# Optimization experiments

Hardware: AMD Instinct MI355X
Metric: run time of the kernel (lower is better)

## Reference

```python
import jax, jax.numpy as jnp
import numpy as np

B, S, D = 8, 2048, 512
EPS = float(jnp.finfo(jnp.float32).eps)  # torch RMSNorm eps=None -> finfo eps


def rmsnorm(x, w):
    var = jnp.mean(jnp.square(x), axis=-1, keepdims=True)
    return x * jax.lax.rsqrt(var + EPS) * w


def setup_inputs() -> dict:
    key = jax.random.key(0)
    ks = jax.random.split(key, 9)
    x = jax.random.normal(ks[0], (B, S, D), dtype=jnp.float32)
    q_expl = jax.random.normal(ks[1], (B, S, D), dtype=jnp.float32)
    k_expl = jax.random.normal(ks[2], (B, S, D), dtype=jnp.float32)
    # parameters (torch Linear: y = x @ W^T + b; store W already transposed [in, out])
    sc1 = 1.0 / np.sqrt(D)
    W1 = jax.random.uniform(ks[3], (D, 2 * D), jnp.float32, -sc1, sc1)
    b1 = jax.random.uniform(ks[4], (2 * D,), jnp.float32, -sc1, sc1)
    W2 = jax.random.uniform(ks[5], (D, D), jnp.float32, -sc1, sc1)
    b2 = jax.random.uniform(ks[6], (D,), jnp.float32, -sc1, sc1)
    norm1_w = jnp.ones((D,), jnp.float32)
    norm2_w = jnp.ones((D,), jnp.float32)
    return {"x": x, "q_expl": q_expl, "k_expl": k_expl,
            "W1": W1, "b1": b1, "W2": W2, "b2": b2,
            "norm1_w": norm1_w, "norm2_w": norm2_w}


def reference(x, q_expl, k_expl, W1, b1, W2, b2, norm1_w, norm2_w):
    d = x.shape[-1]
    # single-head attention: scores [B,S,S]
    scores = jnp.einsum('bqd,bkd->bqk', q_expl, k_expl) / jnp.sqrt(jnp.float32(d))
    attn = jax.nn.softmax(scores, axis=-1)
    attn_out = jnp.einsum('bqk,bkd->bqd', attn, x)
    # dropout is identity in eval mode
    h = rmsnorm(x + attn_out, norm1_w)
    # GeGLU FFN: Linear(D->2D), chunk, gelu(x1)*x2, Linear(D->D)
    proj = h @ W1 + b1
    x1, x2 = jnp.split(proj, 2, axis=-1)
    g = jax.nn.gelu(x1, approximate=False) * x2
    ff = g @ W2 + b2
    return rmsnorm(h + ff, norm2_w)
```

## Files before the change

kernel.cpp:

```cpp
#include <hip/hip_runtime.h>
#include <math.h>

static constexpr float EPS_F = 1.1920929e-07f;
static constexpr float SCL   = 0.044194173824159216f;

typedef __attribute__((ext_vector_type(8))) short  short8;
typedef __attribute__((ext_vector_type(4))) float  floatx4;

__device__ __forceinline__ float4 ld4(const float* p){ return *(const float4*)p; }
__device__ __forceinline__ ushort f2bf(float f){
  union { float f; unsigned u; } v; v.f = f;
  return (ushort)((v.u + 0x7FFFu + ((v.u >> 16) & 1u)) >> 16);
}
__device__ __forceinline__ float bf2f(ushort h){
  union { unsigned u; float f; } v; v.u = ((unsigned)h) << 16;
  return v.f;
}
#define MFMA16(A,B,C) __builtin_amdgcn_mfma_f32_16x16x32_bf16((A),(B),(C),0,0,0)

__device__ __forceinline__ void gld16(void* lds, const void* g){
  __builtin_amdgcn_global_load_lds(
      (const __attribute__((address_space(1))) unsigned int*)g,
      (__attribute__((address_space(3))) unsigned int*)lds, 16, 0, 0);
}


__global__ __launch_bounds__(256)
void prep(const float* __restrict__ q, const float* __restrict__ k,
          const float* __restrict__ x, const float* __restrict__ W1,
          const float* __restrict__ W2,
          ushort* __restrict__ Qb, ushort* __restrict__ Kb,
          ushort* __restrict__ XT, ushort* __restrict__ W1T,
          ushort* __restrict__ W2T)
{
  const int bi = blockIdx.x, t = threadIdx.x;
  if (bi < 8192){
    const size_t i4 = ((size_t)bi*256 + t)*4;
    float4 v = ld4(q + i4);
    ushort4 o;
    o.x=f2bf(v.x*SCL); o.y=f2bf(v.y*SCL); o.z=f2bf(v.z*SCL); o.w=f2bf(v.w*SCL);
    *(ushort4*)(Qb + i4) = o;
    float4 u = ld4(k + i4);
    o.x=f2bf(u.x); o.y=f2bf(u.y); o.z=f2bf(u.z); o.w=f2bf(u.w);
    *(ushort4*)(Kb + i4) = o;
    return;
  }
  const float* in; ushort* out; int R, C, c0, r0; size_t boff;
  if (bi < 10240){
    const int id = bi - 8192;
    in = x; out = XT; R = 2048; C = 512;
    boff = (size_t)(id >> 8) * R * C;
    c0 = (id & 7)*64; r0 = ((id >> 3) & 31)*64;
  } else if (bi < 10368){
    const int id = bi - 10240;
    in = W1; out = W1T; R = 512; C = 1024; boff = 0;
    c0 = (id & 15)*64; r0 = (id >> 4)*64;
  } else {
    const int id = bi - 10368;
    in = W2; out = W2T; R = 512; C = 512; boff = 0;
    c0 = (id & 7)*64; r0 = (id >> 3)*64;
  }
  __shared__ __align__(16) ushort tile[64*68];
#pragma unroll
  for (int it = 0; it < 4; ++it){
    int f = t + it*256, r = f >> 4, c4 = f & 15;
    float4 v = ld4(in + boff + (size_t)(r0+r)*C + c0 + c4*4);
    ushort4 o; o.x=f2bf(v.x); o.y=f2bf(v.y); o.z=f2bf(v.z); o.w=f2bf(v.w);
    *(ushort4*)&tile[r*68 + c4*4] = o;
  }
  __syncthreads();
#pragma unroll
  for (int it = 0; it < 4; ++it){
    int f = t + it*256, c = f >> 4, q4 = f & 15;
    ushort4 o;
    o.x = tile[(q4*4+0)*68 + c];
    o.y = tile[(q4*4+1)*68 + c];
    o.z = tile[(q4*4+2)*68 + c];
    o.w = tile[(q4*4+3)*68 + c];
    *(ushort4*)(out + boff + (size_t)(c0+c)*R + r0 + q4*4) = o;
  }
}

__global__ __launch_bounds__(256)
void qk_gemm(const ushort* __restrict__ Qbf, const ushort* __restrict__ Kbf,
             ushort* __restrict__ scores, float* __restrict__ rowsum)
{
  __shared__ __align__(16) ushort As[2][128*32];
  __shared__ __align__(16) ushort Bs[2][128*32];
  const int t=threadIdx.x, lane=t&63, w=t>>6;
  const int id = blockIdx.x;
  const int b = id & 7, s = id >> 3;
  const int m0 = (s & 15)*128, n0 = (s >> 4)*128;
  const ushort* Qb = Qbf + ((size_t)b*2048 + m0)*512;
  const ushort* Kb = Kbf + ((size_t)b*2048 + n0)*512;
  const int sr = w*32 + (lane>>2), sc = (lane&3)*8;
  const int ga=(w&1)*4, gb2=(w>>1)*4, l15=lane&15, quad=lane>>4;

  floatx4 acc[4][4];
#pragma unroll
  for (int i=0;i<4;++i)
#pragma unroll
    for (int j=0;j<4;++j) acc[i][j]=(floatx4){0.f,0.f,0.f,0.f};

  auto stage = [&](int buf, int k0){
    gld16(&As[buf][(w*32)*32],    Qb + (size_t)sr*512      + k0 + sc);
    gld16(&As[buf][(w*32+16)*32], Qb + (size_t)(sr+16)*512 + k0 + sc);
    gld16(&Bs[buf][(w*32)*32],    Kb + (size_t)sr*512      + k0 + sc);
    gld16(&Bs[buf][(w*32+16)*32], Kb + (size_t)(sr+16)*512 + k0 + sc);
  };

  stage(0, 0);
  for (int kc=0; kc<16; ++kc){
    __syncthreads();
    if (kc < 15) stage((kc+1)&1, (kc+1)*32);
    const ushort* A = As[kc&1];
    const ushort* B = Bs[kc&1];
    short8 af[4], bfr[4];
#pragma unroll
    for (int i=0;i<4;++i) af[i]  = *(const short8*)&A[((ga+i)*16 + l15)*32 + quad*8];
#pragma unroll
    for (int j=0;j<4;++j) bfr[j] = *(const short8*)&B[((gb2+j)*16 + l15)*32 + quad*8];
#pragma unroll
    for (int i=0;i<4;++i)
#pragma unroll
      for (int j=0;j<4;++j)
        acc[i][j] = MFMA16(af[i], bfr[j], acc[i][j]);
  }

  ushort* sb = scores + (size_t)b*2048*2048;
  float rs[4][4];
#pragma unroll
  for (int i=0;i<4;++i)
#pragma unroll
    for (int r=0;r<4;++r) rs[i][r] = 0.f;
#pragma unroll
  for (int i=0;i<4;++i){
    const int rm = m0 + (ga+i)*16 + quad*4;
#pragma unroll
    for (int j=0;j<4;++j){
      const int cn = n0 + (gb2+j)*16 + l15;
#pragma unroll
      for (int r=0;r<4;++r){
        float e = __expf(acc[i][j][r]);
        ushort eb = f2bf(e);
        sb[(size_t)(rm+r)*2048 + cn] = eb;
        rs[i][r] += bf2f(eb);
      }
    }
  }
#pragma unroll
  for (int i=0;i<4;++i)
#pragma unroll
    for (int r=0;r<4;++r){
      float p = rs[i][r];
      p += __shfl_xor(p,1); p += __shfl_xor(p,2);
      p += __shfl_xor(p,4); p += __shfl_xor(p,8);
      if (l15 == 0)
        atomicAdd(&rowsum[(size_t)b*2048 + m0 + (ga+i)*16 + quad*4 + r], p);
    }
}

__global__ __launch_bounds__(256)
void pv128(const ushort* __restrict__ P, const ushort* __restrict__ XT,
           const float* __restrict__ rowsum, ushort* __restrict__ attn)
{
  __shared__ __align__(16) ushort As[2][128*32];
  __shared__ __align__(16) ushort Bs[2][128*32];
  const int t=threadIdx.x, lane=t&63, w=t>>6;
  const int id = blockIdx.x;
  const int b = id & 7, s = id >> 3;
  const int m0 = (s >> 2)*128, n0 = (s & 3)*128;
  const ushort* Pb = P  + ((size_t)b*2048 + m0)*2048;
  const ushort* Xb = XT + ((size_t)b*512  + n0)*2048;
  const int sr = w*32 + (lane>>2), sc = (lane&3)*8;
  const int ga=(w&1)*4, gb2=(w>>1)*4, l15=lane&15, quad=lane>>4;

  floatx4 acc[4][4];
#pragma unroll
  for (int i=0;i<4;++i)
#pragma unroll
    for (int j=0;j<4;++j) acc[i][j]=(floatx4){0.f,0.f,0.f,0.f};

  auto stage = [&](int buf, int k0){
    gld16(&As[buf][(w*32)*32],    Pb + (size_t)sr*2048      + k0 + sc);
    gld16(&As[buf][(w*32+16)*32], Pb + (size_t)(sr+16)*2048 + k0 + sc);
    gld16(&Bs[buf][(w*32)*32],    Xb + (size_t)sr*2048      + k0 + sc);
    gld16(&Bs[buf][(w*32+16)*32], Xb + (size_t)(sr+16)*2048 + k0 + sc);
  };

  stage(0, 0);
  for (int kc=0; kc<64; ++kc){
    __syncthreads();
    if (kc < 63) stage((kc+1)&1, (kc+1)*32);
    const ushort* A = As[kc&1];
    const ushort* B = Bs[kc&1];
    short8 af[4], bfr[4];
#pragma unroll
    for (int i=0;i<4;++i) af[i]  = *(const short8*)&A[((ga+i)*16 + l15)*32 + quad*8];
#pragma unroll
    for (int j=0;j<4;++j) bfr[j] = *(const short8*)&B[((gb2+j)*16 + l15)*32 + quad*8];
#pragma unroll
    for (int i=0;i<4;++i)
#pragma unroll
      for (int j=0;j<4;++j)
        acc[i][j] = MFMA16(af[i], bfr[j], acc[i][j]);
  }

  ushort* ab = attn + (size_t)b*2048*512;
#pragma unroll
  for (int i=0;i<4;++i){
    const int rm = m0 + (ga+i)*16 + quad*4;
    float inv[4];
#pragma unroll
    for (int r=0;r<4;++r)
      inv[r] = 1.0f / rowsum[(size_t)b*2048 + rm + r];
#pragma unroll
    for (int j=0;j<4;++j){
      const int cn = n0 + (gb2+j)*16 + l15;
#pragma unroll
      for (int r=0;r<4;++r)
        ab[(size_t)(rm+r)*512 + cn] = f2bf(acc[i][j][r] * inv[r]);
    }
  }
}

__global__ __launch_bounds__(256)
void res_rms1(const float* __restrict__ x, const float* __restrict__ n1w,
              ushort* __restrict__ ah)
{
  const int wid = threadIdx.x >> 6, lane = threadIdx.x & 63;
  const size_t row = (size_t)blockIdx.x*4 + wid;
  ushort* ar = ah + row*512;
  const float* xr = x + row*512;
  ushort4 a0 = *(const ushort4*)&ar[lane*8];
  ushort4 a1 = *(const ushort4*)&ar[lane*8 + 4];
  float4 x0 = ld4(xr + lane*8), x1 = ld4(xr + lane*8 + 4);
  float h[8];
  h[0]=x0.x+bf2f(a0.x); h[1]=x0.y+bf2f(a0.y); h[2]=x0.z+bf2f(a0.z); h[3]=x0.w+bf2f(a0.w);
  h[4]=x1.x+bf2f(a1.x); h[5]=x1.y+bf2f(a1.y); h[6]=x1.z+bf2f(a1.z); h[7]=x1.w+bf2f(a1.w);
  float ss = 0.f;
#pragma unroll
  for (int e=0;e<8;++e) ss += h[e]*h[e];
#pragma unroll
  for (int s=1;s<64;s<<=1) ss += __shfl_xor(ss, s);
  const float rr = rsqrtf(ss*(1.0f/512.0f) + EPS_F);
  ushort4 o0, o1;
  o0.x=f2bf(h[0]*rr*n1w[lane*8+0]); o0.y=f2bf(h[1]*rr*n1w[lane*8+1]);
  o0.z=f2bf(h[2]*rr*n1w[lane*8+2]); o0.w=f2bf(h[3]*rr*n1w[lane*8+3]);
  o1.x=f2bf(h[4]*rr*n1w[lane*8+4]); o1.y=f2bf(h[5]*rr*n1w[lane*8+5]);
  o1.z=f2bf(h[6]*rr*n1w[lane*8+6]); o1.w=f2bf(h[7]*rr*n1w[lane*8+7]);
  *(ushort4*)&ar[lane*8]     = o0;
  *(ushort4*)&ar[lane*8 + 4] = o1;
}

__global__ __launch_bounds__(256)
void ffn1(const ushort* __restrict__ hbf, const ushort* __restrict__ W1T,
          const float* __restrict__ b1, ushort* __restrict__ gbuf)
{
  __shared__ __align__(16) ushort As[2][128*32];
  __shared__ __align__(16) ushort Bs[2][128*32];
  const int t=threadIdx.x, lane=t&63, w=t>>6;
  const int id = blockIdx.x;
  const int xcd = id & 7, sl = id >> 3;
  const int m0 = (xcd*16 + (sl>>3))*128, n0 = (sl & 7)*64;
  const int sr = w*32 + (lane>>2), sc=(lane&3)*8;
  const int ga=(w&1)*4, b2w=(w>>1);
  const int l15=lane&15, quad=lane>>4;
  const int gr0 = (sr < 64) ? (n0+sr) : (448+n0+sr);
  const int sr1 = sr+16;
  const int gr1 = (sr1 < 64) ? (n0+sr1) : (448+n0+sr1);

  floatx4 acc[4][4];
#pragma unroll
  for (int i=0;i<4;++i)
#pragma unroll
    for (int j=0;j<4;++j) acc[i][j]=(floatx4){0.f,0.f,0.f,0.f};

  auto stage = [&](int buf, int k0){
    gld16(&As[buf][(w*32)*32],    hbf + (size_t)(m0+sr)*512  + k0 + sc);
    gld16(&As[buf][(w*32+16)*32], hbf + (size_t)(m0+sr1)*512 + k0 + sc);
    gld16(&Bs[buf][(w*32)*32],    W1T + (size_t)gr0*512 + k0 + sc);
    gld16(&Bs[buf][(w*32+16)*32], W1T + (size_t)gr1*512 + k0 + sc);
  };

  stage(0, 0);
  for (int kc=0; kc<16; ++kc){
    __syncthreads();
    if (kc < 15) stage((kc+1)&1, (kc+1)*32);
    const ushort* A = As[kc&1];
    const ushort* B = Bs[kc&1];
    short8 af[4], bfr[4];
#pragma unroll
    for (int i=0;i<4;++i) af[i] = *(const short8*)&A[((ga+i)*16 + l15)*32 + quad*8];
#pragma unroll
    for (int jj=0;jj<4;++jj){
      const int g1 = (jj<2) ? (b2w*2+jj) : (4 + b2w*2 + (jj-2));
      bfr[jj] = *(const short8*)&B[(g1*16 + l15)*32 + quad*8];
    }
#pragma unroll
    for (int i=0;i<4;++i)
#pragma unroll
      for (int jj=0;jj<4;++jj)
        acc[i][jj] = MFMA16(af[i], bfr[jj], acc[i][jj]);
  }

#pragma unroll
  for (int i=0;i<4;++i){
#pragma unroll
    for (int jj=0;jj<2;++jj){
      const int col = n0 + (b2w*2+jj)*16 + l15;
      const float bb1 = b1[col], bb2 = b1[512+col];
#pragma unroll
      for (int r=0;r<4;++r){
        const int row = m0 + (ga+i)*16 + quad*4 + r;
        float x1 = acc[i][jj][r]   + bb1;
        float x2 = acc[i][jj+2][r] + bb2;
        float gl = 0.5f*x1*(1.0f + erff(x1*0.70710678118654752f));
        gbuf[(size_t)row*512 + col] = f2bf(gl*x2);
      }
    }
  }
}

__global__ __launch_bounds__(256)
void ff128(const ushort* __restrict__ gb, const ushort* __restrict__ W2T,
           ushort* __restrict__ ff)
{
  __shared__ __align__(16) ushort As[2][128*32];
  __shared__ __align__(16) ushort Bs[2][128*32];
  const int t=threadIdx.x, lane=t&63, w=t>>6;
  const int id = blockIdx.x;
  const int xcd = id & 7, sl = id >> 3;
  const int m0 = (xcd*16 + (sl>>2))*128, n0 = (sl & 3)*128;
  const ushort* Ab = gb  + (size_t)m0*512;
  const ushort* Bb = W2T + (size_t)n0*512;
  const int sr = w*32 + (lane>>2), sc = (lane&3)*8;
  const int ga=(w&1)*4, gb2=(w>>1)*4, l15=lane&15, quad=lane>>4;

  floatx4 acc[4][4];
#pragma unroll
  for (int i=0;i<4;++i)
#pragma unroll
    for (int j=0;j<4;++j) acc[i][j]=(floatx4){0.f,0.f,0.f,0.f};

  auto stage = [&](int buf, int k0){
    gld16(&As[buf][(w*32)*32],    Ab + (size_t)sr*512      + k0 + sc);
    gld16(&As[buf][(w*32+16)*32], Ab + (size_t)(sr+16)*512 + k0 + sc);
    gld16(&Bs[buf][(w*32)*32],    Bb + (size_t)sr*512      + k0 + sc);
    gld16(&Bs[buf][(w*32+16)*32], Bb + (size_t)(sr+16)*512 + k0 + sc);
  };

  stage(0, 0);
  for (int kc=0; kc<16; ++kc){
    __syncthreads();
    if (kc < 15) stage((kc+1)&1, (kc+1)*32);
    const ushort* A = As[kc&1];
    const ushort* B = Bs[kc&1];
    short8 af[4], bfr[4];
#pragma unroll
    for (int i=0;i<4;++i) af[i]  = *(const short8*)&A[((ga+i)*16 + l15)*32 + quad*8];
#pragma unroll
    for (int j=0;j<4;++j) bfr[j] = *(const short8*)&B[((gb2+j)*16 + l15)*32 + quad*8];
#pragma unroll
    for (int i=0;i<4;++i)
#pragma unroll
      for (int j=0;j<4;++j)
        acc[i][j] = MFMA16(af[i], bfr[j], acc[i][j]);
  }

#pragma unroll
  for (int i=0;i<4;++i){
    const int rm = m0 + (ga+i)*16 + quad*4;
#pragma unroll
    for (int j=0;j<4;++j){
      const int cn = n0 + (gb2+j)*16 + l15;
#pragma unroll
      for (int r=0;r<4;++r)
        ff[(size_t)(rm+r)*512 + cn] = f2bf(acc[i][j][r]);
    }
  }
}

__global__ __launch_bounds__(256)
void res_rms2(const ushort* __restrict__ hbf, const ushort* __restrict__ ff,
              const float* __restrict__ b2, const float* __restrict__ n2w,
              float* __restrict__ out)
{
  const int wid = threadIdx.x >> 6, lane = threadIdx.x & 63;
  const size_t row = (size_t)blockIdx.x*4 + wid;
  const ushort* hr = hbf + row*512;
  const ushort* fr = ff  + row*512;
  ushort4 h0 = *(const ushort4*)&hr[lane*8];
  ushort4 h1 = *(const ushort4*)&hr[lane*8 + 4];
  ushort4 f0 = *(const ushort4*)&fr[lane*8];
  ushort4 f1 = *(const ushort4*)&fr[lane*8 + 4];
  float4 bb0 = ld4(b2 + lane*8), bb1 = ld4(b2 + lane*8 + 4);
  float y[8];
  y[0]=bf2f(h0.x)+bf2f(f0.x)+bb0.x; y[1]=bf2f(h0.y)+bf2f(f0.y)+bb0.y;
  y[2]=bf2f(h0.z)+bf2f(f0.z)+bb0.z; y[3]=bf2f(h0.w)+bf2f(f0.w)+bb0.w;
  y[4]=bf2f(h1.x)+bf2f(f1.x)+bb1.x; y[5]=bf2f(h1.y)+bf2f(f1.y)+bb1.y;
  y[6]=bf2f(h1.z)+bf2f(f1.z)+bb1.z; y[7]=bf2f(h1.w)+bf2f(f1.w)+bb1.w;
  float ss = 0.f;
#pragma unroll
  for (int e=0;e<8;++e) ss += y[e]*y[e];
#pragma unroll
  for (int s=1;s<64;s<<=1) ss += __shfl_xor(ss, s);
  const float rr = rsqrtf(ss*(1.0f/512.0f) + EPS_F);
  float4 w0 = ld4(n2w + lane*8), w1 = ld4(n2w + lane*8 + 4);
  float* orow = out + row*512;
  float4 o0, o1;
  o0.x=y[0]*rr*w0.x; o0.y=y[1]*rr*w0.y; o0.z=y[2]*rr*w0.z; o0.w=y[3]*rr*w0.w;
  o1.x=y[4]*rr*w1.x; o1.y=y[5]*rr*w1.y; o1.z=y[6]*rr*w1.z; o1.w=y[7]*rr*w1.w;
  *(float4*)(orow + lane*8)     = o0;
  *(float4*)(orow + lane*8 + 4) = o1;
}

extern "C" void kernel_launch(void* const* d_in, const int* in_sizes, int n_in,
                              void* d_out, int out_size, void* d_ws, size_t ws_size,
                              hipStream_t stream)
{
  const float* x   = (const float*)d_in[0];
  const float* q   = (const float*)d_in[1];
  const float* k   = (const float*)d_in[2];
  const float* W1  = (const float*)d_in[3];
  const float* b1  = (const float*)d_in[4];
  const float* W2  = (const float*)d_in[5];
  const float* b2  = (const float*)d_in[6];
  const float* n1w = (const float*)d_in[7];
  const float* n2w = (const float*)d_in[8];
  float* out = (float*)d_out;

  ushort* scoresP = (ushort*)d_ws;
  ushort* XT  = scoresP + (size_t)8*2048*2048;
  ushort* Qbf = XT  + (size_t)8*512*2048;
  ushort* Kbf = Qbf + (size_t)8*2048*512;
  ushort* W1T = Kbf + (size_t)8*2048*512;
  ushort* W2T = W1T + (size_t)1024*512;
  float*  rowsum = (float*)(W2T + (size_t)512*512);
  ushort* attn = Qbf;
  ushort* hbf  = Qbf;
  ushort* gbuf = Kbf;
  ushort* ffb  = scoresP;

  hipMemsetAsync(rowsum, 0, (size_t)8*2048*sizeof(float), stream);
  prep     <<<dim3(10432),  256, 0, stream>>>(q, k, x, W1, W2, Qbf, Kbf, XT, W1T, W2T);
  qk_gemm  <<<dim3(2048),   256, 0, stream>>>(Qbf, Kbf, scoresP, rowsum);
  pv128    <<<dim3(512),    256, 0, stream>>>(scoresP, XT, rowsum, attn);
  res_rms1 <<<dim3(4096),   256, 0, stream>>>(x, n1w, hbf);
  ffn1     <<<dim3(1024),   256, 0, stream>>>(hbf, W1T, b1, gbuf);
  ff128    <<<dim3(512),    256, 0, stream>>>(gbuf, W2T, ffb);
  res_rms2 <<<dim3(4096),   256, 0, stream>>>(hbf, ffb, b2, n2w, out);
}
```

Before: 340.8 us.

## Replace QK GEMM with 256x256-tile, 8-wave kernel using swizzled LDS pipeline

Replaces the 128x128-tile QK^T kernel with a 256x256-tile kernel of 512 threads (8 waves), each wave computing a 128x64 sub-tile, with a 64-wide K step and 128 KB of dynamic LDS. LDS rows are XOR-swizzled to avoid bank conflicts, and loads for the next tiles are issued in phases inside the MFMA loop, with explicit waitcnt, barriers and setprio. The goal is more operand reuse per byte loaded and better overlap of global loads with MFMA work. The cost is one block per CU, because of the large LDS footprint, and heavier register pressure from 32 accumulator tiles per wave.

```diff
diff --git a/kernel.cpp b/kernel.cpp
--- a/kernel.cpp
+++ b/kernel.cpp
@@ -23,7 +23,6 @@
       (const __attribute__((address_space(1))) unsigned int*)g,
       (__attribute__((address_space(3))) unsigned int*)lds, 16, 0, 0);
 }
-
 
 __global__ __launch_bounds__(256)
 void prep(const float* __restrict__ q, const float* __restrict__ k,
@@ -81,83 +80,120 @@
   }
 }
 
-__global__ __launch_bounds__(256)
-void qk_gemm(const ushort* __restrict__ Qbf, const ushort* __restrict__ Kbf,
-             ushort* __restrict__ scores, float* __restrict__ rowsum)
-{
-  __shared__ __align__(16) ushort As[2][128*32];
-  __shared__ __align__(16) ushort Bs[2][128*32];
-  const int t=threadIdx.x, lane=t&63, w=t>>6;
+__global__ __launch_bounds__(512)
+void qk8(const ushort* __restrict__ Qbf, const ushort* __restrict__ Kbf,
+         ushort* __restrict__ scores, float* __restrict__ rowsum)
+{
+  extern __shared__ __align__(16) ushort smem[];
+  const int t = threadIdx.x, lane = t & 63, w = t >> 6;
   const int id = blockIdx.x;
   const int b = id & 7, s = id >> 3;
-  const int m0 = (s & 15)*128, n0 = (s >> 4)*128;
-  const ushort* Qb = Qbf + ((size_t)b*2048 + m0)*512;
-  const ushort* Kb = Kbf + ((size_t)b*2048 + n0)*512;
-  const int sr = w*32 + (lane>>2), sc = (lane&3)*8;
-  const int ga=(w&1)*4, gb2=(w>>1)*4, l15=lane&15, quad=lane>>4;
-
-  floatx4 acc[4][4];
-#pragma unroll
-  for (int i=0;i<4;++i)
-#pragma unroll
-    for (int j=0;j<4;++j) acc[i][j]=(floatx4){0.f,0.f,0.f,0.f};
-
-  auto stage = [&](int buf, int k0){
-    gld16(&As[buf][(w*32)*32],    Qb + (size_t)sr*512      + k0 + sc);
-    gld16(&As[buf][(w*32+16)*32], Qb + (size_t)(sr+16)*512 + k0 + sc);
-    gld16(&Bs[buf][(w*32)*32],    Kb + (size_t)sr*512      + k0 + sc);
-    gld16(&Bs[buf][(w*32+16)*32], Kb + (size_t)(sr+16)*512 + k0 + sc);
+  const int m0 = (s & 7) * 256, n0 = (s >> 3) * 256;
+  const ushort* Qb = Qbf + ((size_t)b*2048 + (size_t)m0)*512;
+  const ushort* Kb = Kbf + ((size_t)b*2048 + (size_t)n0)*512;
+  const int wr = w >> 2, wc = w & 3;
+  const int l15 = lane & 15, quad = lane >> 4;
+  const int c0  = (quad ^ (l15 & 7)) * 8;
+  const int srow = lane >> 3;
+  const int skc  = ((lane & 7) ^ srow) * 8;
+
+  floatx4 acc[8][4];
+#pragma unroll
+  for (int i = 0; i < 8; ++i)
+#pragma unroll
+    for (int j = 0; j < 4; ++j) acc[i][j] = (floatx4){0.f,0.f,0.f,0.f};
+
+  auto stage = [&](int buf, const ushort* gsrc, int isB, int kt, int h){
+    ushort* base = smem + buf*32768 + isB*16384 + h*8192;
+#pragma unroll
+    for (int r = 0; r < 2; ++r){
+      const int rw = r*8 + w;
+      gld16(base + rw*512,
+            gsrc + (size_t)(h*128 + rw*8 + srow)*512 + kt*64 + skc);
+    }
   };
 
-  stage(0, 0);
-  for (int kc=0; kc<16; ++kc){
-    __syncthreads();
-    if (kc < 15) stage((kc+1)&1, (kc+1)*32);
-    const ushort* A = As[kc&1];
-    const ushort* B = Bs[kc&1];
-    short8 af[4], bfr[4];
-#pragma unroll
-    for (int i=0;i<4;++i) af[i]  = *(const short8*)&A[((ga+i)*16 + l15)*32 + quad*8];
-#pragma unroll
-    for (int j=0;j<4;++j) bfr[j] = *(const short8*)&B[((gb2+j)*16 + l15)*32 + quad*8];
-#pragma unroll
-    for (int i=0;i<4;++i)
-#pragma unroll
-      for (int j=0;j<4;++j)
-        acc[i][j] = MFMA16(af[i], bfr[j], acc[i][j]);
+  stage(0, Qb, 0, 0, 0);
+  stage(0, Qb, 0, 0, 1);
+  stage(0, Kb, 1, 0, 0);
+  stage(0, Kb, 1, 0, 1);
+  stage(1, Kb, 1, 1, 0);
+  stage(1, Kb, 1, 1, 1);
+  asm volatile("s_waitcnt vmcnt(4)" ::: "memory");
+  __builtin_amdgcn_s_barrier();
+
+  short8 af[2][2], bfr[4][2];
+  const int NT = 8;
+
+  for (int kt = 0; kt < NT; ++kt){
+    const int cur = kt & 1;
+    const ushort* A  = smem + cur*32768;
+    const ushort* Bt = A + 16384;
+#pragma unroll
+    for (int p = 0; p < 4; ++p){
+      if (p == 0){
+#pragma unroll
+        for (int ni = 0; ni < 4; ++ni)
+#pragma unroll
+          for (int ks = 0; ks < 2; ++ks)
+            bfr[ni][ks] = *(const short8*)
+              &Bt[(wc*64 + ni*16 + l15)*64 + (c0 ^ (ks*32))];
+      }
+#pragma unroll
+      for (int mi = 0; mi < 2; ++mi)
+#pragma unroll
+        for (int ks = 0; ks < 2; ++ks)
+          af[mi][ks] = *(const short8*)
+            &A[(wr*128 + (p*2 + mi)*16 + l15)*64 + (c0 ^ (ks*32))];
+      if (p == 0 && kt+1 < NT) stage(cur^1, Qb, 0, kt+1, 0);
+      if (p == 1 && kt+1 < NT) stage(cur^1, Qb, 0, kt+1, 1);
+      if (p == 2 && kt+2 < NT) stage(cur,   Kb, 1, kt+2, 0);
+      if (p == 3 && kt+2 < NT) stage(cur,   Kb, 1, kt+2, 1);
+      __builtin_amdgcn_s_barrier();
+      asm volatile("s_waitcnt lgkmcnt(0)" ::: "memory");
+      __builtin_amdgcn_sched_barrier(0);
+      __builtin_amdgcn_s_setprio(1);
+#pragma unroll
+      for (int mi = 0; mi < 2; ++mi)
+#pragma unroll
+        for (int ni = 0; ni < 4; ++ni)
+#pragma unroll
+          for (int ks = 0; ks < 2; ++ks)
+            acc[p*2+mi][ni] = MFMA16(af[mi][ks], bfr[ni][ks], acc[p*2+mi][ni]);
+      __builtin_amdgcn_s_setprio(0);
+      if (p == 3){
+        if (kt + 2 < NT) asm volatile("s_waitcnt vmcnt(4)" ::: "memory");
+        else             asm volatile("s_waitcnt vmcnt(0)" ::: "memory");
+      }
+      __builtin_amdgcn_s_barrier();
+    }
   }
 
   ushort* sb = scores + (size_t)b*2048*2048;
-  float rs[4][4];
-#pragma unroll
-  for (int i=0;i<4;++i)
-#pragma unroll
-    for (int r=0;r<4;++r) rs[i][r] = 0.f;
-#pragma unroll
-  for (int i=0;i<4;++i){
-    const int rm = m0 + (ga+i)*16 + quad*4;
-#pragma unroll
-    for (int j=0;j<4;++j){
-      const int cn = n0 + (gb2+j)*16 + l15;
-#pragma unroll
-      for (int r=0;r<4;++r){
-        float e = __expf(acc[i][j][r]);
+#pragma unroll
+  for (int m = 0; m < 8; ++m){
+    const int rm = m0 + wr*128 + m*16 + quad*4;
+    float rs[4] = {0.f,0.f,0.f,0.f};
+#pragma unroll
+    for (int n = 0; n < 4; ++n){
+      const int cn = n0 + wc*64 + n*16 + l15;
+#pragma unroll
+      for (int r = 0; r < 4; ++r){
+        float e = __expf(acc[m][n][r]);
         ushort eb = f2bf(e);
-        sb[(size_t)(rm+r)*2048 + cn] = eb;
-        rs[i][r] += bf2f(eb);
+        sb[(size_t)(rm + r)*2048 + cn] = eb;
+        rs[r] += bf2f(eb);
       }
     }
-  }
-#pragma unroll
-  for (int i=0;i<4;++i)
-#pragma unroll
-    for (int r=0;r<4;++r){
-      float p = rs[i][r];
-      p += __shfl_xor(p,1); p += __shfl_xor(p,2);
-      p += __shfl_xor(p,4); p += __shfl_xor(p,8);
+#pragma unroll
+    for (int r = 0; r < 4; ++r){
+      float p2 = rs[r];
+      p2 += __shfl_xor(p2, 1); p2 += __shfl_xor(p2, 2);
+      p2 += __shfl_xor(p2, 4); p2 += __shfl_xor(p2, 8);
       if (l15 == 0)
-        atomicAdd(&rowsum[(size_t)b*2048 + m0 + (ga+i)*16 + quad*4 + r], p);
-    }
+        atomicAdd(&rowsum[(size_t)b*2048 + rm + r], p2);
+    }
+  }
 }
 
 __global__ __launch_bounds__(256)
@@ -444,7 +480,7 @@
 
   hipMemsetAsync(rowsum, 0, (size_t)8*2048*sizeof(float), stream);
   prep     <<<dim3(10432),  256, 0, stream>>>(q, k, x, W1, W2, Qbf, Kbf, XT, W1T, W2T);
-  qk_gemm  <<<dim3(2048),   256, 0, stream>>>(Qbf, Kbf, scoresP, rowsum);
+  qk8      <<<dim3(512),    512, 131072, stream>>>(Qbf, Kbf, scoresP, rowsum);
   pv128    <<<dim3(512),    256, 0, stream>>>(scoresP, XT, rowsum, attn);
   res_rms1 <<<dim3(4096),   256, 0, stream>>>(x, n1w, hbf);
   ffn1     <<<dim3(1024),   256, 0, stream>>>(hbf, W1T, b1, gbuf);
```

Result: faster. 324.9 us (-4.7%).
